# Performance work log

Hardware: AMD Instinct MI355X
Metric: run time of the kernel (lower is better)

Reference implementation:

```python
import jax, jax.numpy as jnp
import numpy as np

D = 1024
H = 16
HD = D // H
FF = 4 * D

def layer_norm(x, g, b, eps=1e-5):
    mu = jnp.mean(x, axis=-1, keepdims=True)
    var = jnp.var(x, axis=-1, keepdims=True)
    return (x - mu) * jax.lax.rsqrt(var + eps) * g + b

def setup_inputs() -> dict:
    key = jax.random.key(0)
    ks = jax.random.split(key, 8)
    s = 0.02
    return {
        "x": jax.random.normal(ks[0], (2, 2048, D), jnp.float32),
        "ln1_g": jnp.ones((D,), jnp.float32),
        "ln1_b": jnp.zeros((D,), jnp.float32),
        "w_qkv": jax.random.normal(ks[1], (3 * D, D), jnp.float32) * s,
        "b_qkv": jnp.zeros((3 * D,), jnp.float32),
        "w_proj": jax.random.normal(ks[2], (D, D), jnp.float32) * s,
        "b_proj": jnp.zeros((D,), jnp.float32),
        "ln2_g": jnp.ones((D,), jnp.float32),
        "ln2_b": jnp.zeros((D,), jnp.float32),
        "w_fc1": jax.random.normal(ks[3], (FF, D), jnp.float32) * s,
        "b_fc1": jnp.zeros((FF,), jnp.float32),
        "w_fc2": jax.random.normal(ks[4], (D, FF), jnp.float32) * s,
        "b_fc2": jnp.zeros((D,), jnp.float32),
    }

def reference(x, ln1_g, ln1_b, w_qkv, b_qkv, w_proj, b_proj,
              ln2_g, ln2_b, w_fc1, b_fc1, w_fc2, b_fc2):
    B, N, C = x.shape
    scale = HD ** -0.5
    # --- attention branch (pre-norm) ---
    h = layer_norm(x, ln1_g, ln1_b)
    qkv = h @ w_qkv.T + b_qkv                      # [B,N,3D]
    qkv = qkv.reshape(B, N, 3, H, HD).transpose(2, 0, 3, 1, 4)
    q, k, v = qkv[0], qkv[1], qkv[2]               # [B,H,N,HD]
    attn = jnp.einsum('bhnd,bhmd->bhnm', q, k) * scale
    attn = jax.nn.softmax(attn, axis=-1)
    o = jnp.einsum('bhnm,bhmd->bhnd', attn, v)     # [B,H,N,HD]
    o = o.transpose(0, 2, 1, 3).reshape(B, N, C)
    x = x + (o @ w_proj.T + b_proj)
    # --- FFN branch (pre-norm) ---
    h = layer_norm(x, ln2_g, ln2_b)
    h = jax.nn.gelu(h @ w_fc1.T + b_fc1, approximate=False)
    x = x + (h @ w_fc2.T + b_fc2)
    return x
```

## Files before the change

### kernel.cpp

```cpp
#include <hip/hip_runtime.h>

typedef __attribute__((ext_vector_type(8))) short short8;
typedef __attribute__((ext_vector_type(4))) float f32x4;

static __device__ __forceinline__ unsigned short f2bf(float f){
  unsigned u = __float_as_uint(f);
  u += 0x7FFF + ((u >> 16) & 1);
  return (unsigned short)(u >> 16);
}

static __device__ __forceinline__ f32x4 MF(short8 a, short8 b, f32x4 c){
  return __builtin_amdgcn_mfma_f32_16x16x32_bf16(a, b, c, 0, 0, 0);
}

#define GL16(g, l) __builtin_amdgcn_global_load_lds( \
    (const __attribute__((address_space(1))) void*)(g), \
    (__attribute__((address_space(3))) void*)(l), 16, 0, 0)

#define SBAR { __builtin_amdgcn_sched_barrier(0); __builtin_amdgcn_s_barrier(); __builtin_amdgcn_sched_barrier(0); }

__global__ __launch_bounds__(256) void cvt_all(
    const float* __restrict__ a0, const float* __restrict__ a1,
    const float* __restrict__ a2, const float* __restrict__ a3,
    unsigned short* __restrict__ o0, unsigned short* __restrict__ o1,
    unsigned short* __restrict__ o2, unsigned short* __restrict__ o3){
  int i = blockIdx.x * 256 + threadIdx.x;
  const float* src; unsigned short* dst; int off;
  if (i < 786432)       { src = a0; dst = o0; off = i; }
  else if (i < 1048576) { src = a1; dst = o1; off = i - 786432; }
  else if (i < 2097152) { src = a2; dst = o2; off = i - 1048576; }
  else                  { src = a3; dst = o3; off = i - 2097152; }
  float4 v = reinterpret_cast<const float4*>(src)[off];
  ushort4 o;
  o.x = f2bf(v.x); o.y = f2bf(v.y); o.z = f2bf(v.z); o.w = f2bf(v.w);
  reinterpret_cast<ushort4*>(dst)[off] = o;
}

__global__ __launch_bounds__(256) void ln_bf16(const float* __restrict__ x,
    const float* __restrict__ g, const float* __restrict__ b,
    unsigned short* __restrict__ out){
  int row = blockIdx.x, t = threadIdx.x;
  const float* xr = x + (size_t)row * 1024;
  float4 xv = reinterpret_cast<const float4*>(xr)[t];
  float s  = xv.x + xv.y + xv.z + xv.w;
  float sq = xv.x*xv.x + xv.y*xv.y + xv.z*xv.z + xv.w*xv.w;
  #pragma unroll
  for (int m = 32; m >= 1; m >>= 1){ s += __shfl_xor(s, m); sq += __shfl_xor(sq, m); }
  __shared__ float ss[4], ssq[4];
  int w = t >> 6, lane = t & 63;
  if (lane == 0){ ss[w] = s; ssq[w] = sq; }
  __syncthreads();
  s  = ss[0] + ss[1] + ss[2] + ss[3];
  sq = ssq[0] + ssq[1] + ssq[2] + ssq[3];
  float mu = s * (1.f/1024.f);
  float rs = rsqrtf(sq * (1.f/1024.f) - mu*mu + 1e-5f);
  float4 gv = reinterpret_cast<const float4*>(g)[t];
  float4 bv = reinterpret_cast<const float4*>(b)[t];
  ushort4 o;
  o.x = f2bf((xv.x - mu) * rs * gv.x + bv.x);
  o.y = f2bf((xv.y - mu) * rs * gv.y + bv.y);
  o.z = f2bf((xv.z - mu) * rs * gv.z + bv.z);
  o.w = f2bf((xv.w - mu) * rs * gv.w + bv.w);
  reinterpret_cast<ushort4*>(out + (size_t)row * 1024)[t] = o;
}

template<int EPI>
__global__ __launch_bounds__(512, 2) void gemm8p(
    const unsigned short* __restrict__ A,
    const unsigned short* __restrict__ B,
    const float* __restrict__ bias,
    void* __restrict__ C,
    int M, int N, int K)
{
  __shared__ __attribute__((aligned(16))) short As[2 * 256 * 64];
  __shared__ __attribute__((aligned(16))) short Bs[2 * 256 * 64];
  const int NT = K >> 6;
  int tid = threadIdx.x, lane = tid & 63, wave = tid >> 6;
  int wm = wave >> 2, wn = wave & 3;
  int l15 = lane & 15, hi = lane >> 4;
  int hi2 = hi ^ (((l15 >> 2) & 1) << 1);
  int bm = blockIdx.y * 256, bn = blockIdx.x * 256;
  int lr = lane >> 3;
  int sg8 = ((lane & 7) ^ ((lane >> 5) << 1)) * 8;
  int rb0 = wave * 16;

  f32x4 acc[8][4] = {};
  short8 aR[4][2], bA[2][2], bB[2][2];

  auto stage = [&](int T, int h){
    if (T >= NT) return;
    const unsigned short* src = (h < 2) ? (A + (size_t)(bm + ((h & 1) << 7)) * K)
                                        : (B + (size_t)(bn + ((h & 1) << 7)) * K);
    short* dst = ((h < 2) ? As : Bs) + ((T & 1) << 14) + ((h & 1) << 13);
    const unsigned short* s = src + (size_t)(rb0 + lr) * K + (T << 6) + sg8;
    GL16(s, dst + rb0 * 64);
    GL16(s + (size_t)8 * K, dst + (rb0 + 8) * 64);
  };
  auto LDA = [&](const short* Ab, int m, int kk){
    int R = wm * 128 + m * 16 + l15;
    return *(const short8*)(Ab + R * 64 + kk * 32 + hi2 * 8);
  };
  auto LDB = [&](const short* Bb, int n, int kk){
    int R = wn * 64 + n * 16 + l15;
    return *(const short8*)(Bb + R * 64 + kk * 32 + hi2 * 8);
  };

  stage(0, 0); stage(0, 1); stage(0, 2); stage(0, 3);
  stage(1, 0); stage(1, 1);
  asm volatile("s_waitcnt vmcnt(4)" ::: "memory");
  SBAR;

  for (int i = 0; i < (NT >> 1); ++i){
    int t0 = 2 * i, t1 = t0 + 1;
    const short* A0 = As;            const short* B0 = Bs;
    const short* A1 = As + 16384;    const short* B1 = Bs + 16384;
    #pragma unroll
    for (int m = 0; m < 4; m++){ aR[m][0] = LDA(A0, m, 0); aR[m][1] = LDA(A0, m, 1); }
    #pragma unroll
    for (int n = 0; n < 2; n++){ bA[n][0] = LDB(B0, n, 0); bA[n][1] = LDB(B0, n, 1); }
    __builtin_amdgcn_sched_barrier(0);
    stage(t1, 2);
    SBAR;
    __builtin_amdgcn_s_setprio(1);
    #pragma unroll
    for (int m = 0; m < 4; m++)
      #pragma unroll
      for (int n = 0; n < 2; n++)
        #pragma unroll
        for (int kk = 0; kk < 2; kk++) acc[m][n] = MF(aR[m][kk], bA[n][kk], acc[m][n]);
    __builtin_amdgcn_s_setprio(0);
    SBAR;
    #pragma unroll
    for (int n = 0; n < 2; n++){ bB[n][0] = LDB(B0, n + 2, 0); bB[n][1] = LDB(B0, n + 2, 1); }
    __builtin_amdgcn_sched_barrier(0);
    stage(t1, 3);
    SBAR;
    __builtin_amdgcn_s_setprio(1);
    #pragma unroll
    for (int m = 0; m < 4; m++)
      #pragma unroll
      for (int n = 0; n < 2; n++)
        #pragma unroll
        for (int kk = 0; kk < 2; kk++) acc[m][n + 2] = MF(aR[m][kk], bB[n][kk], acc[m][n + 2]);
    __builtin_amdgcn_s_setprio(0);
    SBAR;
    #pragma unroll
    for (int m = 0; m < 4; m++){ aR[m][0] = LDA(A0, m + 4, 0); aR[m][1] = LDA(A0, m + 4, 1); }
    __builtin_amdgcn_sched_barrier(0);
    stage(t0 + 2, 0);
    SBAR;
    __builtin_amdgcn_s_setprio(1);
    #pragma unroll
    for (int m = 0; m < 4; m++)
      #pragma unroll
      for (int n = 0; n < 2; n++)
        #pragma unroll
        for (int kk = 0; kk < 2; kk++) acc[m + 4][n] = MF(aR[m][kk], bA[n][kk], acc[m + 4][n]);
    __builtin_amdgcn_s_setprio(0);
    SBAR;
    stage(t0 + 2, 1);
    SBAR;
    __builtin_amdgcn_s_setprio(1);
    #pragma unroll
    for (int m = 0; m < 4; m++)
      #pragma unroll
      for (int n = 0; n < 2; n++)
        #pragma unroll
        for (int kk = 0; kk < 2; kk++) acc[m + 4][n + 2] = MF(aR[m][kk], bB[n][kk], acc[m + 4][n + 2]);
    __builtin_amdgcn_s_setprio(0);
    asm volatile("s_waitcnt vmcnt(4)" ::: "memory");
    SBAR;
    #pragma unroll
    for (int m = 0; m < 4; m++){ aR[m][0] = LDA(A1, m, 0); aR[m][1] = LDA(A1, m, 1); }
    #pragma unroll
    for (int n = 0; n < 2; n++){ bA[n][0] = LDB(B1, n, 0); bA[n][1] = LDB(B1, n, 1); }
    __builtin_amdgcn_sched_barrier(0);
    stage(t0 + 2, 2);
    SBAR;
    __builtin_amdgcn_s_setprio(1);
    #pragma unroll
    for (int m = 0; m < 4; m++)
      #pragma unroll
      for (int n = 0; n < 2; n++)
        #pragma unroll
        for (int kk = 0; kk < 2; kk++) acc[m][n] = MF(aR[m][kk], bA[n][kk], acc[m][n]);
    __builtin_amdgcn_s_setprio(0);
    SBAR;
    #pragma unroll
    for (int n = 0; n < 2; n++){ bB[n][0] = LDB(B1, n + 2, 0); bB[n][1] = LDB(B1, n + 2, 1); }
    __builtin_amdgcn_sched_barrier(0);
    stage(t0 + 2, 3);
    SBAR;
    __builtin_amdgcn_s_setprio(1);
    #pragma unroll
    for (int m = 0; m < 4; m++)
      #pragma unroll
      for (int n = 0; n < 2; n++)
        #pragma unroll
        for (int kk = 0; kk < 2; kk++) acc[m][n + 2] = MF(aR[m][kk], bB[n][kk], acc[m][n + 2]);
    __builtin_amdgcn_s_setprio(0);
    SBAR;
    #pragma unroll
    for (int m = 0; m < 4; m++){ aR[m][0] = LDA(A1, m + 4, 0); aR[m][1] = LDA(A1, m + 4, 1); }
    __builtin_amdgcn_sched_barrier(0);
    stage(t0 + 3, 0);
    SBAR;
    __builtin_amdgcn_s_setprio(1);
    #pragma unroll
    for (int m = 0; m < 4; m++)
      #pragma unroll
      for (int n = 0; n < 2; n++)
        #pragma unroll
        for (int kk = 0; kk < 2; kk++) acc[m + 4][n] = MF(aR[m][kk], bA[n][kk], acc[m + 4][n]);
    __builtin_amdgcn_s_setprio(0);
    SBAR;
    stage(t0 + 3, 1);
    SBAR;
    __builtin_amdgcn_s_setprio(1);
    #pragma unroll
    for (int m = 0; m < 4; m++)
      #pragma unroll
      for (int n = 0; n < 2; n++)
        #pragma unroll
        for (int kk = 0; kk < 2; kk++) acc[m + 4][n + 2] = MF(aR[m][kk], bB[n][kk], acc[m + 4][n + 2]);
    __builtin_amdgcn_s_setprio(0);
    asm volatile("s_waitcnt vmcnt(4)" ::: "memory");
    SBAR;
  }

  #pragma unroll
  for (int m = 0; m < 8; m++){
    int row = bm + wm * 128 + m * 16 + hi * 4;
    #pragma unroll
    for (int n = 0; n < 4; n++){
      int col = bn + wn * 64 + n * 16 + l15;
      float bv = bias[col];
      #pragma unroll
      for (int j = 0; j < 4; j++){
        float v = acc[m][n][j] + bv;
        if (EPI == 1){
          float w2 = v * v;
          float t = exp2f(v * fmaf(w2, 0.10294322f, 2.3022078f));
          float r = __builtin_amdgcn_rcpf(1.f + t);
          v = v - v * r;
        }
        ((unsigned short*)C)[(size_t)(row + j) * N + col] = f2bf(v);
      }
    }
  }
}

template<int EPI>
__global__ __launch_bounds__(512) void gemm_bt8(
    const unsigned short* __restrict__ A,
    const unsigned short* __restrict__ B,
    const float* __restrict__ bias,
    const float* __restrict__ resid,
    void* __restrict__ C,
    int M, int N, int K)
{
  __shared__ __attribute__((aligned(16))) short As[2][64 * 64];
  __shared__ __attribute__((aligned(16))) short Bs[2][128 * 64];
  int tid = threadIdx.x;
  int lane = tid & 63, wave = tid >> 6;
  int wm = wave >> 2, wn = wave & 3;
  int l15 = lane & 15, hi = lane >> 4, l7 = l15 & 7;
  int lin = blockIdx.y * 8 + blockIdx.x;
  int xcd = lin & 7, idx = lin >> 3;
  int bm = (xcd * 8 + (idx >> 3)) * 64;
  int bn = (idx & 7) * 128;
  int lr = lane >> 3, lseg = lane & 7;
  int sega = (lseg ^ lr) * 8;
  f32x4 acc[2][2] = {};
  const int NT = K >> 6;
  auto stage = [&](int buf, int k0){
    GL16(A + (size_t)(bm + wave * 8 + lr) * K + k0 + sega, &As[buf][wave * 8 * 64]);
    GL16(B + (size_t)(bn + wave * 16 + lr) * K + k0 + sega, &Bs[buf][wave * 16 * 64]);
    GL16(B + (size_t)(bn + wave * 16 + 8 + lr) * K + k0 + sega, &Bs[buf][(wave * 16 + 8) * 64]);
  };
  stage(0, 0);
  for (int t = 0; t < NT; t++){
    int cur = t & 1;
    if (t + 1 < NT){
      stage(cur ^ 1, (t + 1) << 6);
      asm volatile("s_waitcnt vmcnt(3)" ::: "memory");
    } else {
      asm volatile("s_waitcnt vmcnt(0)" ::: "memory");
    }
    SBAR;
    #pragma unroll
    for (int kk = 0; kk < 2; kk++){
      short8 af[2], bf[2];
      #pragma unroll
      for (int m = 0; m < 2; m++){
        int R = wm * 32 + m * 16 + l15;
        af[m] = *(const short8*)(&As[cur][R * 64 + (((kk << 2) | hi) ^ l7) * 8]);
      }
      #pragma unroll
      for (int n = 0; n < 2; n++){
        int R = wn * 32 + n * 16 + l15;
        bf[n] = *(const short8*)(&Bs[cur][R * 64 + (((kk << 2) | hi) ^ l7) * 8]);
      }
      #pragma unroll
      for (int m = 0; m < 2; m++)
        #pragma unroll
        for (int n = 0; n < 2; n++)
          acc[m][n] = MF(af[m], bf[n], acc[m][n]);
    }
    SBAR;
  }
  #pragma unroll
  for (int m = 0; m < 2; m++){
    int row = bm + wm * 32 + m * 16 + hi * 4;
    #pragma unroll
    for (int n = 0; n < 2; n++){
      int col = bn + wn * 32 + n * 16 + l15;
      float bv = bias[col];
      #pragma unroll
      for (int j = 0; j < 4; j++){
        float v = acc[m][n][j] + bv;
        int r = row + j;
        if (EPI == 2){
          ((float*)C)[(size_t)r * N + col] = v + resid[(size_t)r * N + col];
        } else {
          ((unsigned short*)C)[(size_t)r * N + col] = f2bf(v);
        }
      }
    }
  }
}

__global__ __launch_bounds__(512) void attn_fwd(const unsigned short* __restrict__ qkv,
                                                unsigned short* __restrict__ o){
  __shared__ __attribute__((aligned(16))) short K_lds[2][64*64];
  __shared__ __attribute__((aligned(16))) short V_lds[2][64*64];
  __shared__ __attribute__((aligned(16))) short P_lds[8][16*64];
  int tid = threadIdx.x, wave = tid >> 6, lane = tid & 63;
  int l15 = lane & 15, hi = lane >> 4, l7 = l15 & 7;
  int bid = blockIdx.x;
  int swz = (bid & 7) * 64 + (bid >> 3);
  int qt = swz & 15, bh = swz >> 4;
  int b = bh >> 4, h = bh & 15;
  const unsigned short* qbase = qkv + (size_t)b * 2048 * 3072 + h * 64;
  const unsigned short* kbase = qbase + 1024;
  const unsigned short* vbase = qbase + 2048;
  int qrow = qt * 128 + wave * 16 + l15;
  short8 qf0 = *(const short8*)(qbase + (size_t)qrow * 3072 + hi * 8);
  short8 qf1 = *(const short8*)(qbase + (size_t)qrow * 3072 + 32 + hi * 8);
  #pragma unroll
  for (int j = 0; j < 8; j++){
    float q0 = __uint_as_float((unsigned)(unsigned short)qf0[j] << 16) * 0.18033688f;
    float q1 = __uint_as_float((unsigned)(unsigned short)qf1[j] << 16) * 0.18033688f;
    qf0[j] = (short)f2bf(q0);
    qf1[j] = (short)f2bf(q1);
  }
  short8 ones8;
  #pragma unroll
  for (int j = 0; j < 8; j++) ones8[j] = (short)0x3F80;
  int krow = tid >> 3, kseg = tid & 7;
  int vt = tid - 256;
  int kp = vt & 31, ds8 = (vt >> 5) & 7;
  int vcg = kp >> 2, vwi = (2 * kp) & 7;
  f32x4 accO[4] = {};
  f32x4 lacc = {};
  short* Pw = &P_lds[wave][0];

  {
    short8 kv = *(const short8*)(kbase + (size_t)krow * 3072 + kseg * 8);
    short8 vv0, vv1;
    if (vt >= 0){
      const unsigned short* vr = vbase + (size_t)(2 * kp) * 3072 + ds8 * 8;
      vv0 = *(const short8*)vr; vv1 = *(const short8*)(vr + 3072);
    }
    *(short8*)(&K_lds[0][krow * 64 + ((kseg ^ (krow & 7)) << 3)]) = kv;
    if (vt >= 0){
      unsigned* Vw = (unsigned*)&V_lds[0][0];
      #pragma unroll
      for (int j = 0; j < 8; j++){
        int d = ds8 * 8 + j;
        int sa = d * 64 + ((vcg ^ (d & 7)) << 3) + vwi;
        Vw[sa >> 1] = (unsigned)(unsigned short)vv0[j] | ((unsigned)(unsigned short)vv1[j] << 16);
      }
    }
    __syncthreads();
  }

  for (int t = 0; t < 32; t++){
    int cur = t & 1;
    const short* Kc = &K_lds[cur][0];
    const short* Vc = &V_lds[cur][0];
    short8 kv, vv0, vv1;
    if (t < 31){
      int kt = (t + 1) * 64;
      kv = *(const short8*)(kbase + (size_t)(kt + krow) * 3072 + kseg * 8);
      if (vt >= 0){
        const unsigned short* vr = vbase + (size_t)(kt + 2 * kp) * 3072 + ds8 * 8;
        vv0 = *(const short8*)vr; vv1 = *(const short8*)(vr + 3072);
      }
    }
    f32x4 sacc[4];
    __builtin_amdgcn_s_setprio(1);
    #pragma unroll
    for (int kb = 0; kb < 4; kb++){
      f32x4 s = {};
      short8 ka = *(const short8*)(Kc + (kb * 16 + l15) * 64 + ((hi ^ l7) << 3));
      s = __builtin_amdgcn_mfma_f32_16x16x32_bf16(ka, qf0, s, 0, 0, 0);
      short8 kb_ = *(const short8*)(Kc + (kb * 16 + l15) * 64 + (((4 + hi) ^ l7) << 3));
      s = __builtin_amdgcn_mfma_f32_16x16x32_bf16(kb_, qf1, s, 0, 0, 0);
      sacc[kb] = s;
    }
    __builtin_amdgcn_s_setprio(0);
    unsigned pu[8];
    #pragma unroll
    for (int kb = 0; kb < 4; kb++){
      unsigned u0 = (unsigned)(int)fmaf(sacc[kb][0], 128.f, 16248.6f);
      unsigned u1 = (unsigned)(int)fmaf(sacc[kb][1], 128.f, 16248.6f);
      unsigned u2 = (unsigned)(int)fmaf(sacc[kb][2], 128.f, 16248.6f);
      unsigned u3 = (unsigned)(int)fmaf(sacc[kb][3], 128.f, 16248.6f);
      pu[kb * 2]     = u0 | (u1 << 16);
      pu[kb * 2 + 1] = u2 | (u3 << 16);
    }
    #pragma unroll
    for (int kb = 0; kb < 4; kb++){
      int sa = l15 * 64 + ((((kb << 1) | (hi >> 1)) ^ l7) << 3) + ((hi & 1) << 2);
      *(uint2*)(Pw + sa) = make_uint2(pu[kb * 2], pu[kb * 2 + 1]);
    }
    __builtin_amdgcn_s_setprio(1);
    #pragma unroll
    for (int kb2 = 0; kb2 < 2; kb2++){
      short8 pf = *(const short8*)(Pw + l15 * 64 + ((((kb2 << 2) | hi) ^ l7) << 3));
      #pragma unroll
      for (int db = 0; db < 4; db++){
        short8 vf = *(const short8*)(Vc + (db * 16 + l15) * 64 + ((((kb2 << 2) | hi) ^ l7) << 3));
        accO[db] = __builtin_amdgcn_mfma_f32_16x16x32_bf16(vf, pf, accO[db], 0, 0, 0);
      }
      lacc = __builtin_amdgcn_mfma_f32_16x16x32_bf16(ones8, pf, lacc, 0, 0, 0);
    }
    __builtin_amdgcn_s_setprio(0);
    if (t < 31){
      int nxt = cur ^ 1;
      *(short8*)(&K_lds[nxt][krow * 64 + ((kseg ^ (krow & 7)) << 3)]) = kv;
      if (vt >= 0){
        unsigned* Vw = (unsigned*)&V_lds[nxt][0];
        #pragma unroll
        for (int j = 0; j < 8; j++){
          int d = ds8 * 8 + j;
          int sa = d * 64 + ((vcg ^ (d & 7)) << 3) + vwi;
          Vw[sa >> 1] = (unsigned)(unsigned short)vv0[j] | ((unsigned)(unsigned short)vv1[j] << 16);
        }
      }
      __syncthreads();
    }
  }
  float inv = 1.f / lacc[0];
  unsigned short* ob = o + (size_t)(b * 2048 + qt * 128 + wave * 16 + l15) * 1024 + h * 64;
  #pragma unroll
  for (int db = 0; db < 4; db++){
    ushort4 w;
    w.x = f2bf(accO[db][0] * inv);
    w.y = f2bf(accO[db][1] * inv);
    w.z = f2bf(accO[db][2] * inv);
    w.w = f2bf(accO[db][3] * inv);
    *(ushort4*)(ob + db * 16 + hi * 4) = w;
  }
}

extern "C" void kernel_launch(void* const* d_in, const int* in_sizes, int n_in,
                              void* d_out, int out_size, void* d_ws, size_t ws_size,
                              hipStream_t stream){
  const float* x      = (const float*)d_in[0];
  const float* ln1_g  = (const float*)d_in[1];
  const float* ln1_b  = (const float*)d_in[2];
  const float* w_qkv  = (const float*)d_in[3];
  const float* b_qkv  = (const float*)d_in[4];
  const float* w_proj = (const float*)d_in[5];
  const float* b_proj = (const float*)d_in[6];
  const float* ln2_g  = (const float*)d_in[7];
  const float* ln2_b  = (const float*)d_in[8];
  const float* w_fc1  = (const float*)d_in[9];
  const float* b_fc1  = (const float*)d_in[10];
  const float* w_fc2  = (const float*)d_in[11];
  const float* b_fc2  = (const float*)d_in[12];
  float* out = (float*)d_out;
  char* ws = (char*)d_ws;
  const size_t MB = 1024 * 1024;
  unsigned short* h     = (unsigned short*)(ws);
  unsigned short* qkv   = (unsigned short*)(ws + 8*MB);
  unsigned short* ob    = (unsigned short*)(ws + 32*MB);
  float*          x1    = (float*)(ws + 40*MB);
  unsigned short* f     = (unsigned short*)(ws + 56*MB);
  unsigned short* wqkvb = (unsigned short*)(ws + 88*MB);
  unsigned short* wprojb= (unsigned short*)(ws + 94*MB);
  unsigned short* wfc1b = (unsigned short*)(ws + 96*MB);
  unsigned short* wfc2b = (unsigned short*)(ws + 104*MB);

  cvt_all<<<12288, 256, 0, stream>>>(w_qkv, w_proj, w_fc1, w_fc2,
                                     wqkvb, wprojb, wfc1b, wfc2b);

  ln_bf16<<<4096, 256, 0, stream>>>(x, ln1_g, ln1_b, h);
  gemm8p<0><<<dim3(12, 16), 512, 0, stream>>>(h, wqkvb, b_qkv, qkv, 4096, 3072, 1024);
  attn_fwd<<<512, 512, 0, stream>>>(qkv, ob);
  gemm_bt8<2><<<dim3(8, 64), 512, 0, stream>>>(ob, wprojb, b_proj, x, x1, 4096, 1024, 1024);
  ln_bf16<<<4096, 256, 0, stream>>>(x1, ln2_g, ln2_b, h);
  gemm8p<1><<<dim3(16, 16), 512, 0, stream>>>(h, wfc1b, b_fc1, f, 4096, 4096, 1024);
  gemm_bt8<2><<<dim3(8, 64), 512, 0, stream>>>(f, wfc2b, b_fc2, x1, out, 4096, 1024, 4096);
}
```

Measured before the change: 220.5 us.

## Use 128x128 ping-pong pipelined GEMM for proj and fc2 with residual epilogue

Replaces the 64x128-tile residual GEMM used for the output projection and FC2 with a 128x128-tile kernel. The new kernel splits global-to-LDS staging into quarter-tile chunks interleaved between MFMA phases, raises wave priority around the MFMA blocks, and sets launch bounds for two blocks per CU. The larger tile raises arithmetic intensity and the software pipeline is meant to hide load latency. The cost is a halved grid (256 blocks), which may underfill the CUs, plus higher register and LDS use per block.

```diff
diff --git a/kernel.cpp b/kernel.cpp
--- a/kernel.cpp
+++ b/kernel.cpp
@@ -251,7 +251,7 @@
 }
 
 template<int EPI>
-__global__ __launch_bounds__(512) void gemm_bt8(
+__global__ __launch_bounds__(512, 2) void gemm8p128(
     const unsigned short* __restrict__ A,
     const unsigned short* __restrict__ B,
     const float* __restrict__ bias,
@@ -259,59 +259,146 @@
     void* __restrict__ C,
     int M, int N, int K)
 {
-  __shared__ __attribute__((aligned(16))) short As[2][64 * 64];
+  __shared__ __attribute__((aligned(16))) short As[2][128 * 64];
   __shared__ __attribute__((aligned(16))) short Bs[2][128 * 64];
-  int tid = threadIdx.x;
-  int lane = tid & 63, wave = tid >> 6;
+  const int NT = K >> 6;
+  int tid = threadIdx.x, lane = tid & 63, wave = tid >> 6;
   int wm = wave >> 2, wn = wave & 3;
   int l15 = lane & 15, hi = lane >> 4, l7 = l15 & 7;
   int lin = blockIdx.y * 8 + blockIdx.x;
   int xcd = lin & 7, idx = lin >> 3;
-  int bm = (xcd * 8 + (idx >> 3)) * 64;
+  int bm = (xcd * 4 + (idx >> 3)) * 128;
   int bn = (idx & 7) * 128;
-  int lr = lane >> 3, lseg = lane & 7;
-  int sega = (lseg ^ lr) * 8;
-  f32x4 acc[2][2] = {};
-  const int NT = K >> 6;
-  auto stage = [&](int buf, int k0){
-    GL16(A + (size_t)(bm + wave * 8 + lr) * K + k0 + sega, &As[buf][wave * 8 * 64]);
-    GL16(B + (size_t)(bn + wave * 16 + lr) * K + k0 + sega, &Bs[buf][wave * 16 * 64]);
-    GL16(B + (size_t)(bn + wave * 16 + 8 + lr) * K + k0 + sega, &Bs[buf][(wave * 16 + 8) * 64]);
+  int lr = lane >> 3;
+  int sega = ((lane & 7) ^ lr) * 8;
+  f32x4 acc[4][2] = {};
+  short8 aR[4][2], bf0[2], bf1[2];
+
+  auto stage = [&](int T, int h){
+    if (T >= NT) return;
+    const unsigned short* src = (h < 2) ? (A + (size_t)bm * K) : (B + (size_t)bn * K);
+    short* dst = ((h < 2) ? &As[0][0] : &Bs[0][0]) + (T & 1) * (128 * 64);
+    int row = ((h & 1) << 6) + wave * 8;
+    GL16(src + (size_t)(row + lr) * K + (T << 6) + sega, dst + row * 64);
   };
-  stage(0, 0);
-  for (int t = 0; t < NT; t++){
-    int cur = t & 1;
-    if (t + 1 < NT){
-      stage(cur ^ 1, (t + 1) << 6);
-      asm volatile("s_waitcnt vmcnt(3)" ::: "memory");
-    } else {
-      asm volatile("s_waitcnt vmcnt(0)" ::: "memory");
-    }
-    SBAR;
-    #pragma unroll
-    for (int kk = 0; kk < 2; kk++){
-      short8 af[2], bf[2];
-      #pragma unroll
-      for (int m = 0; m < 2; m++){
-        int R = wm * 32 + m * 16 + l15;
-        af[m] = *(const short8*)(&As[cur][R * 64 + (((kk << 2) | hi) ^ l7) * 8]);
-      }
-      #pragma unroll
-      for (int n = 0; n < 2; n++){
-        int R = wn * 32 + n * 16 + l15;
-        bf[n] = *(const short8*)(&Bs[cur][R * 64 + (((kk << 2) | hi) ^ l7) * 8]);
-      }
-      #pragma unroll
-      for (int m = 0; m < 2; m++)
-        #pragma unroll
-        for (int n = 0; n < 2; n++)
-          acc[m][n] = MF(af[m], bf[n], acc[m][n]);
-    }
-    SBAR;
-  }
+  auto LDA = [&](const short* Ab, int m, int kk){
+    int R = wm * 64 + m * 16 + l15;
+    return *(const short8*)(Ab + R * 64 + (((kk << 2) | hi) ^ l7) * 8);
+  };
+  auto LDB = [&](const short* Bb, int n, int kk){
+    int R = wn * 32 + n * 16 + l15;
+    return *(const short8*)(Bb + R * 64 + (((kk << 2) | hi) ^ l7) * 8);
+  };
+
+  stage(0, 0); stage(0, 1); stage(0, 2); stage(0, 3);
+  stage(1, 0); stage(1, 1);
+  asm volatile("s_waitcnt vmcnt(2)" ::: "memory");
+  SBAR;
+
+  const short* A0 = &As[0][0]; const short* B0 = &Bs[0][0];
+  const short* A1 = &As[1][0]; const short* B1 = &Bs[1][0];
+
+  for (int i = 0; i < (NT >> 1) - 1; ++i){
+    int t0 = 2 * i, t1 = t0 + 1;
+    #pragma unroll
+    for (int m = 0; m < 4; m++){ aR[m][0] = LDA(A0, m, 0); aR[m][1] = LDA(A0, m, 1); }
+    bf0[0] = LDB(B0, 0, 0); bf0[1] = LDB(B0, 0, 1);
+    __builtin_amdgcn_sched_barrier(0);
+    stage(t1, 2); stage(t1, 3);
+    SBAR;
+    __builtin_amdgcn_s_setprio(1);
+    #pragma unroll
+    for (int m = 0; m < 4; m++)
+      #pragma unroll
+      for (int kk = 0; kk < 2; kk++) acc[m][0] = MF(aR[m][kk], bf0[kk], acc[m][0]);
+    __builtin_amdgcn_s_setprio(0);
+    SBAR;
+    bf1[0] = LDB(B0, 1, 0); bf1[1] = LDB(B0, 1, 1);
+    __builtin_amdgcn_sched_barrier(0);
+    stage(t0 + 2, 0); stage(t0 + 2, 1);
+    SBAR;
+    __builtin_amdgcn_s_setprio(1);
+    #pragma unroll
+    for (int m = 0; m < 4; m++)
+      #pragma unroll
+      for (int kk = 0; kk < 2; kk++) acc[m][1] = MF(aR[m][kk], bf1[kk], acc[m][1]);
+    __builtin_amdgcn_s_setprio(0);
+    asm volatile("s_waitcnt vmcnt(2)" ::: "memory");
+    SBAR;
+    #pragma unroll
+    for (int m = 0; m < 4; m++){ aR[m][0] = LDA(A1, m, 0); aR[m][1] = LDA(A1, m, 1); }
+    bf0[0] = LDB(B1, 0, 0); bf0[1] = LDB(B1, 0, 1);
+    __builtin_amdgcn_sched_barrier(0);
+    stage(t0 + 2, 2); stage(t0 + 2, 3);
+    SBAR;
+    __builtin_amdgcn_s_setprio(1);
+    #pragma unroll
+    for (int m = 0; m < 4; m++)
+      #pragma unroll
+      for (int kk = 0; kk < 2; kk++) acc[m][0] = MF(aR[m][kk], bf0[kk], acc[m][0]);
+    __builtin_amdgcn_s_setprio(0);
+    SBAR;
+    bf1[0] = LDB(B1, 1, 0); bf1[1] = LDB(B1, 1, 1);
+    __builtin_amdgcn_sched_barrier(0);
+    stage(t0 + 3, 0); stage(t0 + 3, 1);
+    SBAR;
+    __builtin_amdgcn_s_setprio(1);
+    #pragma unroll
+    for (int m = 0; m < 4; m++)
+      #pragma unroll
+      for (int kk = 0; kk < 2; kk++) acc[m][1] = MF(aR[m][kk], bf1[kk], acc[m][1]);
+    __builtin_amdgcn_s_setprio(0);
+    asm volatile("s_waitcnt vmcnt(2)" ::: "memory");
+    SBAR;
+  }
+  {
+    #pragma unroll
+    for (int m = 0; m < 4; m++){ aR[m][0] = LDA(A0, m, 0); aR[m][1] = LDA(A0, m, 1); }
+    bf0[0] = LDB(B0, 0, 0); bf0[1] = LDB(B0, 0, 1);
+    __builtin_amdgcn_sched_barrier(0);
+    int t1 = NT - 1;
+    stage(t1, 2); stage(t1, 3);
+    SBAR;
+    __builtin_amdgcn_s_setprio(1);
+    #pragma unroll
+    for (int m = 0; m < 4; m++)
+      #pragma unroll
+      for (int kk = 0; kk < 2; kk++) acc[m][0] = MF(aR[m][kk], bf0[kk], acc[m][0]);
+    __builtin_amdgcn_s_setprio(0);
+    SBAR;
+    bf1[0] = LDB(B0, 1, 0); bf1[1] = LDB(B0, 1, 1);
+    SBAR;
+    __builtin_amdgcn_s_setprio(1);
+    #pragma unroll
+    for (int m = 0; m < 4; m++)
+      #pragma unroll
+      for (int kk = 0; kk < 2; kk++) acc[m][1] = MF(aR[m][kk], bf1[kk], acc[m][1]);
+    __builtin_amdgcn_s_setprio(0);
+    asm volatile("s_waitcnt vmcnt(0)" ::: "memory");
+    SBAR;
+    #pragma unroll
+    for (int m = 0; m < 4; m++){ aR[m][0] = LDA(A1, m, 0); aR[m][1] = LDA(A1, m, 1); }
+    bf0[0] = LDB(B1, 0, 0); bf0[1] = LDB(B1, 0, 1);
+    SBAR;
+    __builtin_amdgcn_s_setprio(1);
+    #pragma unroll
+    for (int m = 0; m < 4; m++)
+      #pragma unroll
+      for (int kk = 0; kk < 2; kk++) acc[m][0] = MF(aR[m][kk], bf0[kk], acc[m][0]);
+    __builtin_amdgcn_s_setprio(0);
+    SBAR;
+    bf1[0] = LDB(B1, 1, 0); bf1[1] = LDB(B1, 1, 1);
+    __builtin_amdgcn_s_setprio(1);
+    #pragma unroll
+    for (int m = 0; m < 4; m++)
+      #pragma unroll
+      for (int kk = 0; kk < 2; kk++) acc[m][1] = MF(aR[m][kk], bf1[kk], acc[m][1]);
+    __builtin_amdgcn_s_setprio(0);
+  }
+
   #pragma unroll
-  for (int m = 0; m < 2; m++){
-    int row = bm + wm * 32 + m * 16 + hi * 4;
+  for (int m = 0; m < 4; m++){
+    int row = bm + wm * 64 + m * 16 + hi * 4;
     #pragma unroll
     for (int n = 0; n < 2; n++){
       int col = bn + wn * 32 + n * 16 + l15;
@@ -500,8 +587,8 @@
   ln_bf16<<<4096, 256, 0, stream>>>(x, ln1_g, ln1_b, h);
   gemm8p<0><<<dim3(12, 16), 512, 0, stream>>>(h, wqkvb, b_qkv, qkv, 4096, 3072, 1024);
   attn_fwd<<<512, 512, 0, stream>>>(qkv, ob);
-  gemm_bt8<2><<<dim3(8, 64), 512, 0, stream>>>(ob, wprojb, b_proj, x, x1, 4096, 1024, 1024);
+  gemm8p128<2><<<dim3(8, 32), 512, 0, stream>>>(ob, wprojb, b_proj, x, x1, 4096, 1024, 1024);
   ln_bf16<<<4096, 256, 0, stream>>>(x1, ln2_g, ln2_b, h);
   gemm8p<1><<<dim3(16, 16), 512, 0, stream>>>(h, wfc1b, b_fc1, f, 4096, 4096, 1024);
-  gemm_bt8<2><<<dim3(8, 64), 512, 0, stream>>>(f, wfc2b, b_fc2, x1, out, 4096, 1024, 4096);
-}
+  gemm8p128<2><<<dim3(8, 32), 512, 0, stream>>>(f, wfc2b, b_fc2, x1, out, 4096, 1024, 4096);
+}
```

Result: no change. 221.8 us (+0.6%).

## Enlarge proj/fc2 GEMM tiles to 128x128 with 4 waves; rebalance attention K/V loads

Applied to the files above, without the earlier changes.

The N=1024 GEMMs (proj and fc2) move from 64x128 tiles on 8 waves to 128x128 tiles on 4 waves, each wave computing a 64x64 sub-tile with 16 MFMAs per k-step under raised priority. This raises arithmetic intensity per LDS fragment load and halves the grid to 256 blocks, at the cost of fewer waves per block and fewer blocks to fill the GPU. Separately, the attention kernel now splits K and V loading between the two halves of the block, with each thread loading two 16-byte chunks. Previously every thread loaded a K chunk and half the threads also loaded V, so the load work was uneven.

```diff
diff --git a/kernel.cpp b/kernel.cpp
--- a/kernel.cpp
+++ b/kernel.cpp
@@ -251,7 +251,7 @@
 }
 
 template<int EPI>
-__global__ __launch_bounds__(512) void gemm_bt8(
+__global__ __launch_bounds__(256) void gemm4w128(
     const unsigned short* __restrict__ A,
     const unsigned short* __restrict__ B,
     const float* __restrict__ bias,
@@ -259,62 +259,70 @@
     void* __restrict__ C,
     int M, int N, int K)
 {
-  __shared__ __attribute__((aligned(16))) short As[2][64 * 64];
+  __shared__ __attribute__((aligned(16))) short As[2][128 * 64];
   __shared__ __attribute__((aligned(16))) short Bs[2][128 * 64];
-  int tid = threadIdx.x;
-  int lane = tid & 63, wave = tid >> 6;
-  int wm = wave >> 2, wn = wave & 3;
+  const int NT = K >> 6;
+  int tid = threadIdx.x, lane = tid & 63, wave = tid >> 6;
+  int wm = wave >> 1, wn = wave & 1;
   int l15 = lane & 15, hi = lane >> 4, l7 = l15 & 7;
   int lin = blockIdx.y * 8 + blockIdx.x;
   int xcd = lin & 7, idx = lin >> 3;
-  int bm = (xcd * 8 + (idx >> 3)) * 64;
+  int bm = (xcd * 4 + (idx >> 3)) * 128;
   int bn = (idx & 7) * 128;
-  int lr = lane >> 3, lseg = lane & 7;
-  int sega = (lseg ^ lr) * 8;
-  f32x4 acc[2][2] = {};
-  const int NT = K >> 6;
+  int lr = lane >> 3;
+  int sega = ((lane & 7) ^ lr) * 8;
+  f32x4 acc[4][4] = {};
+
   auto stage = [&](int buf, int k0){
-    GL16(A + (size_t)(bm + wave * 8 + lr) * K + k0 + sega, &As[buf][wave * 8 * 64]);
-    GL16(B + (size_t)(bn + wave * 16 + lr) * K + k0 + sega, &Bs[buf][wave * 16 * 64]);
-    GL16(B + (size_t)(bn + wave * 16 + 8 + lr) * K + k0 + sega, &Bs[buf][(wave * 16 + 8) * 64]);
-  };
+    #pragma unroll
+    for (int j = 0; j < 4; j++){
+      int row = wave * 32 + j * 8;
+      GL16(A + (size_t)(bm + row + lr) * K + k0 + sega, &As[buf][row * 64]);
+      GL16(B + (size_t)(bn + row + lr) * K + k0 + sega, &Bs[buf][row * 64]);
+    }
+  };
+  auto LDA = [&](int buf, int m, int kk){
+    int R = wm * 64 + m * 16 + l15;
+    return *(const short8*)(&As[buf][R * 64 + (((kk << 2) | hi) ^ l7) * 8]);
+  };
+  auto LDB = [&](int buf, int n, int kk){
+    int R = wn * 64 + n * 16 + l15;
+    return *(const short8*)(&Bs[buf][R * 64 + (((kk << 2) | hi) ^ l7) * 8]);
+  };
+
   stage(0, 0);
   for (int t = 0; t < NT; t++){
     int cur = t & 1;
     if (t + 1 < NT){
       stage(cur ^ 1, (t + 1) << 6);
-      asm volatile("s_waitcnt vmcnt(3)" ::: "memory");
+      asm volatile("s_waitcnt vmcnt(8)" ::: "memory");
     } else {
       asm volatile("s_waitcnt vmcnt(0)" ::: "memory");
     }
     SBAR;
     #pragma unroll
     for (int kk = 0; kk < 2; kk++){
-      short8 af[2], bf[2];
-      #pragma unroll
-      for (int m = 0; m < 2; m++){
-        int R = wm * 32 + m * 16 + l15;
-        af[m] = *(const short8*)(&As[cur][R * 64 + (((kk << 2) | hi) ^ l7) * 8]);
-      }
-      #pragma unroll
-      for (int n = 0; n < 2; n++){
-        int R = wn * 32 + n * 16 + l15;
-        bf[n] = *(const short8*)(&Bs[cur][R * 64 + (((kk << 2) | hi) ^ l7) * 8]);
-      }
-      #pragma unroll
-      for (int m = 0; m < 2; m++)
-        #pragma unroll
-        for (int n = 0; n < 2; n++)
+      short8 af[4], bf[4];
+      #pragma unroll
+      for (int m = 0; m < 4; m++) af[m] = LDA(cur, m, kk);
+      #pragma unroll
+      for (int n = 0; n < 4; n++) bf[n] = LDB(cur, n, kk);
+      __builtin_amdgcn_s_setprio(1);
+      #pragma unroll
+      for (int m = 0; m < 4; m++)
+        #pragma unroll
+        for (int n = 0; n < 4; n++)
           acc[m][n] = MF(af[m], bf[n], acc[m][n]);
+      __builtin_amdgcn_s_setprio(0);
     }
     SBAR;
   }
   #pragma unroll
-  for (int m = 0; m < 2; m++){
-    int row = bm + wm * 32 + m * 16 + hi * 4;
-    #pragma unroll
-    for (int n = 0; n < 2; n++){
-      int col = bn + wn * 32 + n * 16 + l15;
+  for (int m = 0; m < 4; m++){
+    int row = bm + wm * 64 + m * 16 + hi * 4;
+    #pragma unroll
+    for (int n = 0; n < 4; n++){
+      int col = bn + wn * 64 + n * 16 + l15;
       float bv = bias[col];
       #pragma unroll
       for (int j = 0; j < 4; j++){
@@ -357,31 +365,45 @@
   short8 ones8;
   #pragma unroll
   for (int j = 0; j < 8; j++) ones8[j] = (short)0x3F80;
-  int krow = tid >> 3, kseg = tid & 7;
   int vt = tid - 256;
+  int ki0 = tid * 2, ki1 = ki0 + 1;
+  int kr0 = ki0 >> 3, ks0 = ki0 & 7;
+  int kr1 = ki1 >> 3, ks1 = ki1 & 7;
   int kp = vt & 31, ds8 = (vt >> 5) & 7;
   int vcg = kp >> 2, vwi = (2 * kp) & 7;
   f32x4 accO[4] = {};
   f32x4 lacc = {};
   short* Pw = &P_lds[wave][0];
 
-  {
-    short8 kv = *(const short8*)(kbase + (size_t)krow * 3072 + kseg * 8);
-    short8 vv0, vv1;
-    if (vt >= 0){
-      const unsigned short* vr = vbase + (size_t)(2 * kp) * 3072 + ds8 * 8;
-      vv0 = *(const short8*)vr; vv1 = *(const short8*)(vr + 3072);
-    }
-    *(short8*)(&K_lds[0][krow * 64 + ((kseg ^ (krow & 7)) << 3)]) = kv;
-    if (vt >= 0){
-      unsigned* Vw = (unsigned*)&V_lds[0][0];
+  auto kv_load = [&](int kt, short8& s0, short8& s1){
+    if (vt < 0){
+      s0 = *(const short8*)(kbase + (size_t)(kt + kr0) * 3072 + ks0 * 8);
+      s1 = *(const short8*)(kbase + (size_t)(kt + kr1) * 3072 + ks1 * 8);
+    } else {
+      const unsigned short* vr = vbase + (size_t)(kt + 2 * kp) * 3072 + ds8 * 8;
+      s0 = *(const short8*)vr;
+      s1 = *(const short8*)(vr + 3072);
+    }
+  };
+  auto kv_store = [&](int buf, short8 s0, short8 s1){
+    if (vt < 0){
+      *(short8*)(&K_lds[buf][kr0 * 64 + ((ks0 ^ (kr0 & 7)) << 3)]) = s0;
+      *(short8*)(&K_lds[buf][kr1 * 64 + ((ks1 ^ (kr1 & 7)) << 3)]) = s1;
+    } else {
+      unsigned* Vw = (unsigned*)&V_lds[buf][0];
       #pragma unroll
       for (int j = 0; j < 8; j++){
         int d = ds8 * 8 + j;
         int sa = d * 64 + ((vcg ^ (d & 7)) << 3) + vwi;
-        Vw[sa >> 1] = (unsigned)(unsigned short)vv0[j] | ((unsigned)(unsigned short)vv1[j] << 16);
+        Vw[sa >> 1] = (unsigned)(unsigned short)s0[j] | ((unsigned)(unsigned short)s1[j] << 16);
       }
     }
+  };
+
+  {
+    short8 s0, s1;
+    kv_load(0, s0, s1);
+    kv_store(0, s0, s1);
     __syncthreads();
   }
 
@@ -389,15 +411,8 @@
     int cur = t & 1;
     const short* Kc = &K_lds[cur][0];
     const short* Vc = &V_lds[cur][0];
-    short8 kv, vv0, vv1;
-    if (t < 31){
-      int kt = (t + 1) * 64;
-      kv = *(const short8*)(kbase + (size_t)(kt + krow) * 3072 + kseg * 8);
-      if (vt >= 0){
-        const unsigned short* vr = vbase + (size_t)(kt + 2 * kp) * 3072 + ds8 * 8;
-        vv0 = *(const short8*)vr; vv1 = *(const short8*)(vr + 3072);
-      }
-    }
+    short8 s0, s1;
+    if (t < 31) kv_load((t + 1) * 64, s0, s1);
     f32x4 sacc[4];
     __builtin_amdgcn_s_setprio(1);
     #pragma unroll
@@ -438,17 +453,7 @@
     }
     __builtin_amdgcn_s_setprio(0);
     if (t < 31){
-      int nxt = cur ^ 1;
-      *(short8*)(&K_lds[nxt][krow * 64 + ((kseg ^ (krow & 7)) << 3)]) = kv;
-      if (vt >= 0){
-        unsigned* Vw = (unsigned*)&V_lds[nxt][0];
-        #pragma unroll
-        for (int j = 0; j < 8; j++){
-          int d = ds8 * 8 + j;
-          int sa = d * 64 + ((vcg ^ (d & 7)) << 3) + vwi;
-          Vw[sa >> 1] = (unsigned)(unsigned short)vv0[j] | ((unsigned)(unsigned short)vv1[j] << 16);
-        }
-      }
+      kv_store(cur ^ 1, s0, s1);
       __syncthreads();
     }
   }
@@ -500,8 +505,8 @@
   ln_bf16<<<4096, 256, 0, stream>>>(x, ln1_g, ln1_b, h);
   gemm8p<0><<<dim3(12, 16), 512, 0, stream>>>(h, wqkvb, b_qkv, qkv, 4096, 3072, 1024);
   attn_fwd<<<512, 512, 0, stream>>>(qkv, ob);
-  gemm_bt8<2><<<dim3(8, 64), 512, 0, stream>>>(ob, wprojb, b_proj, x, x1, 4096, 1024, 1024);
+  gemm4w128<2><<<dim3(8, 32), 256, 0, stream>>>(ob, wprojb, b_proj, x, x1, 4096, 1024, 1024);
   ln_bf16<<<4096, 256, 0, stream>>>(x1, ln2_g, ln2_b, h);
   gemm8p<1><<<dim3(16, 16), 512, 0, stream>>>(h, wfc1b, b_fc1, f, 4096, 4096, 1024);
-  gemm_bt8<2><<<dim3(8, 64), 512, 0, stream>>>(f, wfc2b, b_fc2, x1, out, 4096, 1024, 4096);
-}
+  gemm4w128<2><<<dim3(8, 32), 256, 0, stream>>>(f, wfc2b, b_fc2, x1, out, 4096, 1024, 4096);
+}
```

Measured after the change: 242.9 us. +10.2%, slower.
